# Kernel tuning notes

Measured on AMD Instinct MI355X. Metric: run time of the kernel, lower is better.

Reference implementation:

```python
import jax, jax.numpy as jnp
import numpy as np

B, S, IN_F, OUT_F = 4, 2048, 4096, 4096

def setup_inputs() -> dict:
    key = jax.random.key(0)
    k1, k2, k3 = jax.random.split(key, 3)
    # int8 activations and weights (symmetric range)
    x = jax.random.randint(k1, (B, S, IN_F), -128, 128, dtype=jnp.int32).astype(jnp.int8)
    weight_q = jax.random.randint(k2, (OUT_F, IN_F), -128, 128, dtype=jnp.int32).astype(jnp.int8)
    scale_x = jnp.float32(0.05)   # activation quant scale
    scale_w = jnp.float32(0.02)   # weight quant scale (scalar, per-tensor)
    scale_y = jax.random.uniform(k3, (OUT_F,), minval=0.5, maxval=2.0, dtype=jnp.float32)  # per-output-row scale
    return {"x": x, "weight_q": weight_q, "scale_x": scale_x, "scale_w": scale_w, "scale_y": scale_y}

def reference(x, weight_q, scale_x, scale_w, scale_y):
    # int8 GEMM with int32 accumulation: [B,S,IN] @ [OUT,IN]^T -> [B,S,OUT]
    acc = jax.lax.dot_general(x, weight_q, ((((2,), (1,)), ((), ()))),
                              preferred_element_type=jnp.int32)
    # fused requantization scale: scale_x * scale_w / scale_y  -> [OUT]
    requant_scale = (scale_x * scale_w / scale_y).astype(jnp.float32)
    out_f = acc.astype(jnp.float32) * requant_scale  # broadcast over last dim
    out_q = jnp.clip(jnp.round(out_f), -128, 127).astype(jnp.int8)
    return out_q, scale_y
```

## Files before the change

### kernel.cpp

```cpp
#include <hip/hip_runtime.h>
#include <cstdint>


#define MDIM 8192
#define NDIM 4096
#define KDIM 4096
#define BM 256
#define BN 256
#define NH 64

typedef int v4i __attribute__((ext_vector_type(4)));

#define FENCE() asm volatile("" ::: "memory")
#define BARX()                    \
  do {                            \
    FENCE();                      \
    __builtin_amdgcn_s_barrier(); \
    FENCE();                      \
  } while (0)
#define LGKM0() asm volatile("s_waitcnt lgkmcnt(0)" ::: "memory")
#define VMCNT4() asm volatile("s_waitcnt vmcnt(4)" ::: "memory")
#define VMCNT0() asm volatile("s_waitcnt vmcnt(0)" ::: "memory")

__device__ __forceinline__ uint32_t pack4(int a, int b, int c, int d) {
  return (uint32_t)(a & 0xFF) | ((uint32_t)(b & 0xFF) << 8) |
         ((uint32_t)(c & 0xFF) << 16) | ((uint32_t)(d & 0xFF) << 24);
}

__global__ __launch_bounds__(256) void pack_kernel(
    const int* __restrict__ x32, const int* __restrict__ w32,
    const float* __restrict__ sy, uint8_t* __restrict__ x8f,
    uint8_t* __restrict__ w8f, float* __restrict__ tail) {
  const int t = blockIdx.x * 256 + threadIdx.x;
  if (t < NDIM) tail[t] = sy[t];
  const int NXC = (MDIM / 16) * KDIM;
  const int NWC = (NDIM / 16) * KDIM;
  if (t >= NXC + NWC) return;
  const int* src;
  uint8_t* dst;
  int chunk;
  if (t < NXC) {
    chunk = t;
    src = x32;
    dst = x8f;
  } else {
    chunk = t - NXC;
    src = w32;
    dst = w8f;
  }
  const int lpos = chunk & 63;
  const int rf = (chunk >> 6) & 15;
  const int h = (chunk >> 10) & 63;
  const int mb = chunk >> 16;
  const int kl = lpos >> 4, fr = lpos & 15;
  const int r = mb * 256 + rf * 16 + fr;
  const int k0 = h * 64 + kl * 16;
  const int* s = src + (size_t)r * KDIM + k0;
  v4i a0 = *(const v4i*)(s + 0);
  v4i a1 = *(const v4i*)(s + 4);
  v4i a2 = *(const v4i*)(s + 8);
  v4i a3 = *(const v4i*)(s + 12);
  v4i o;
  o[0] = (int)pack4(a0[0], a0[1], a0[2], a0[3]);
  o[1] = (int)pack4(a1[0], a1[1], a1[2], a1[3]);
  o[2] = (int)pack4(a2[0], a2[1], a2[2], a2[3]);
  o[3] = (int)pack4(a3[0], a3[1], a3[2], a3[3]);
  *(v4i*)(dst + (size_t)chunk * 16) = o;
}

__global__ __launch_bounds__(512, 2) void gemm_kernel(
    const uint8_t* __restrict__ A8, const uint8_t* __restrict__ B8,
    const float* __restrict__ sxp, const float* __restrict__ swp,
    const float* __restrict__ syp, float* __restrict__ out) {
  __shared__ __align__(16) uint8_t lds[65536];

  const int tid = threadIdx.x;
  const int lane = tid & 63;
  const int wave = tid >> 6;

  const int wg = ((int)blockIdx.x % 8) * 64 + (int)blockIdx.x / 8;
  const int mb = wg >> 4;
  const int nb = wg & 15;

  const int wm2 = wave >> 2;
  const int wn4 = wave & 3;

  const uint8_t* Abase = A8 + ((size_t)mb << 20);
  const uint8_t* Bbase = B8 + ((size_t)nb << 20);

  const uint32_t tid16 = (uint32_t)tid * 16;
  const uint32_t lane16 = (uint32_t)lane * 16;
  const uint32_t aoff = ((uint32_t)(wm2 * 8) << 10) + lane16;
  const uint32_t boff = 16384u + ((uint32_t)(wn4 * 4) << 10) + lane16;

  v4i acc[8][4];
#pragma unroll
  for (int i = 0; i < 8; i++)
#pragma unroll
    for (int j = 0; j < 4; j++) acc[i][j] = (v4i){0, 0, 0, 0};

  auto gload = [&](const uint8_t* src, uint32_t ldsoff) {
    __builtin_amdgcn_global_load_lds(
        (const __attribute__((address_space(1))) void*)src,
        (__attribute__((address_space(3))) void*)(lds + ldsoff), 16, 0, 0);
  };
  auto stage = [&](int h) {
    const uint32_t lb = (uint32_t)(h & 1) * 32768u;
    const uint8_t* sa = Abase + ((size_t)h << 14) + tid16;
    const uint8_t* sb = Bbase + ((size_t)h << 14) + tid16;
    gload(sa, lb + tid16);
    gload(sa + 8192, lb + 8192u + tid16);
    gload(sb, lb + 16384u + tid16);
    gload(sb + 8192, lb + 24576u + tid16);
  };

  v4i af0[8], bf0[4], af1[8], bf1[4];

#define READ_FRAGS(AF, BF, SB)                                   \
  do {                                                           \
    _Pragma("unroll") for (int i = 0; i < 8; i++) AF[i] =        \
        *(const v4i*)(lds + (SB) + aoff + (i << 10));            \
    _Pragma("unroll") for (int j = 0; j < 4; j++) BF[j] =        \
        *(const v4i*)(lds + (SB) + boff + (j << 10));            \
  } while (0)

#define MFMA32(AF, BF)                                                        \
  do {                                                                        \
    _Pragma("unroll") for (int i = 0; i < 8; i++) _Pragma(                    \
        "unroll") for (int j = 0; j < 4; j++) acc[i][j] =                     \
        __builtin_amdgcn_mfma_i32_16x16x64_i8(AF[i], BF[j], acc[i][j], 0, 0, \
                                              0);                             \
  } while (0)

  stage(0);
  stage(1);
  VMCNT4();
  BARX();
  READ_FRAGS(af0, bf0, 0u);

  for (int h = 0; h < 62; h += 2) {
    LGKM0();
    BARX();
    stage(h + 2);
    VMCNT4();
    BARX();
    READ_FRAGS(af1, bf1, 32768u);
    MFMA32(af0, bf0);

    LGKM0();
    BARX();
    stage(h + 3);
    VMCNT4();
    BARX();
    READ_FRAGS(af0, bf0, 0u);
    MFMA32(af1, bf1);
  }

  LGKM0();
  BARX();
  VMCNT0();
  BARX();
  READ_FRAGS(af1, bf1, 32768u);
  MFMA32(af0, bf0);
  MFMA32(af1, bf1);

  const float s = sxp[0] * swp[0];
  const int kl = lane >> 4;
  const int fr = lane & 15;
  const int wrow = mb * 256 + wm2 * 128;
  const int wcol = nb * 256 + wn4 * 64;
#pragma unroll
  for (int j = 0; j < 4; j++) {
    const int col = wcol + j * 16 + fr;
    const float rs = s / syp[col];
#pragma unroll
    for (int i = 0; i < 8; i++) {
      const int row0 = wrow + i * 16 + kl * 4;
#pragma unroll
      for (int r = 0; r < 4; r++) {
        float v = rintf((float)acc[i][j][r] * rs);
        v = fminf(127.f, fmaxf(-128.f, v));
        out[(size_t)(row0 + r) * NDIM + col] = v;
      }
    }
  }
}

extern "C" void kernel_launch(void* const* d_in, const int* in_sizes, int n_in,
                              void* d_out, int out_size, void* d_ws, size_t ws_size,
                              hipStream_t stream) {
  const int* x32 = (const int*)d_in[0];
  const int* w32 = (const int*)d_in[1];
  const float* sx = (const float*)d_in[2];
  const float* sw = (const float*)d_in[3];
  const float* sy = (const float*)d_in[4];
  float* out = (float*)d_out;
  float* tail = out + (size_t)MDIM * NDIM;

  uint8_t* x8f = (uint8_t*)d_ws;
  uint8_t* w8f = x8f + (size_t)MDIM * KDIM;

  const int total = (MDIM / 16) * KDIM + (NDIM / 16) * KDIM;
  pack_kernel<<<total / 256, 256, 0, stream>>>(x32, w32, sy, x8f, w8f, tail);

  const int nblocks = (MDIM / BM) * (NDIM / BN);
  gemm_kernel<<<nblocks, 512, 0, stream>>>(x8f, w8f, sx, sw, sy, out);
}
```

Baseline: 184.2 us.

## Load A fragments directly from global to registers, pipeline B through four LDS stages

```diff
diff --git a/kernel.cpp b/kernel.cpp
--- a/kernel.cpp
+++ b/kernel.cpp
@@ -5,8 +5,6 @@
 #define MDIM 8192
 #define NDIM 4096
 #define KDIM 4096
-#define BM 256
-#define BN 256
 #define NH 64
 
 typedef int v4i __attribute__((ext_vector_type(4)));
@@ -18,9 +16,6 @@
     __builtin_amdgcn_s_barrier(); \
     FENCE();                      \
   } while (0)
-#define LGKM0() asm volatile("s_waitcnt lgkmcnt(0)" ::: "memory")
-#define VMCNT4() asm volatile("s_waitcnt vmcnt(4)" ::: "memory")
-#define VMCNT0() asm volatile("s_waitcnt vmcnt(0)" ::: "memory")
 
 __device__ __forceinline__ uint32_t pack4(int a, int b, int c, int d) {
   return (uint32_t)(a & 0xFF) | ((uint32_t)(b & 0xFF) << 8) |
@@ -85,13 +80,13 @@
   const int wm2 = wave >> 2;
   const int wn4 = wave & 3;
 
-  const uint8_t* Abase = A8 + ((size_t)mb << 20);
-  const uint8_t* Bbase = B8 + ((size_t)nb << 20);
+  const uint8_t* Apan = A8 + ((size_t)mb << 20) +
+                        ((uint32_t)(wm2 * 8) << 10) + (uint32_t)lane * 16;
+  const uint8_t* Bpan = B8 + ((size_t)nb << 20);
 
   const uint32_t tid16 = (uint32_t)tid * 16;
   const uint32_t lane16 = (uint32_t)lane * 16;
-  const uint32_t aoff = ((uint32_t)(wm2 * 8) << 10) + lane16;
-  const uint32_t boff = 16384u + ((uint32_t)(wn4 * 4) << 10) + lane16;
+  const uint32_t boff = ((uint32_t)(wn4 * 4) << 10) + lane16;
 
   v4i acc[8][4];
 #pragma unroll
@@ -104,65 +99,62 @@
         (const __attribute__((address_space(1))) void*)src,
         (__attribute__((address_space(3))) void*)(lds + ldsoff), 16, 0, 0);
   };
-  auto stage = [&](int h) {
-    const uint32_t lb = (uint32_t)(h & 1) * 32768u;
-    const uint8_t* sa = Abase + ((size_t)h << 14) + tid16;
-    const uint8_t* sb = Bbase + ((size_t)h << 14) + tid16;
-    gload(sa, lb + tid16);
-    gload(sa + 8192, lb + 8192u + tid16);
-    gload(sb, lb + 16384u + tid16);
-    gload(sb + 8192, lb + 24576u + tid16);
-  };
-
-  v4i af0[8], bf0[4], af1[8], bf1[4];
-
-#define READ_FRAGS(AF, BF, SB)                                   \
-  do {                                                           \
-    _Pragma("unroll") for (int i = 0; i < 8; i++) AF[i] =        \
-        *(const v4i*)(lds + (SB) + aoff + (i << 10));            \
-    _Pragma("unroll") for (int j = 0; j < 4; j++) BF[j] =        \
-        *(const v4i*)(lds + (SB) + boff + (j << 10));            \
-  } while (0)
+  auto stageB = [&](int h) {
+    const uint32_t s = ((uint32_t)h & 3u) * 16384u;
+    const uint8_t* src = Bpan + ((size_t)h << 14) + tid16;
+    gload(src, s + tid16);
+    gload(src + 8192, s + 8192u + tid16);
+  };
+  auto loadA = [&](v4i(&a)[8], int h) {
+    const uint8_t* p = Apan + ((size_t)h << 14);
+#pragma unroll
+    for (int i = 0; i < 8; i++) a[i] = *(const v4i*)(p + (i << 10));
+  };
+  auto readB = [&](v4i(&b)[4], int h) {
+    const uint8_t* L = lds + ((uint32_t)h & 3u) * 16384u + boff;
+#pragma unroll
+    for (int j = 0; j < 4; j++) b[j] = *(const v4i*)(L + (j << 10));
+  };
 
 #define MFMA32(AF, BF)                                                        \
   do {                                                                        \
     _Pragma("unroll") for (int i = 0; i < 8; i++) _Pragma(                    \
         "unroll") for (int j = 0; j < 4; j++) acc[i][j] =                     \
-        __builtin_amdgcn_mfma_i32_16x16x64_i8(AF[i], BF[j], acc[i][j], 0, 0, \
+        __builtin_amdgcn_mfma_i32_16x16x64_i8(AF[i], BF[j], acc[i][j], 0, 0,  \
                                               0);                             \
   } while (0)
 
-  stage(0);
-  stage(1);
-  VMCNT4();
+  v4i aX[8], aY[8], bX[4], bY[4];
+
+  stageB(0);
+  stageB(1);
+  stageB(2);
+  loadA(aX, 0);
+  asm volatile("s_waitcnt vmcnt(12)" ::: "memory");
   BARX();
-  READ_FRAGS(af0, bf0, 0u);
+  readB(bX, 0);
 
   for (int h = 0; h < 62; h += 2) {
-    LGKM0();
+    asm volatile("s_waitcnt vmcnt(10)" ::: "memory");
     BARX();
-    stage(h + 2);
-    VMCNT4();
+    stageB(h + 3);
+    loadA(aY, h + 1);
+    readB(bY, h + 1);
+    MFMA32(aX, bX);
+
+    asm volatile("s_waitcnt vmcnt(10)" ::: "memory");
     BARX();
-    READ_FRAGS(af1, bf1, 32768u);
-    MFMA32(af0, bf0);
-
-    LGKM0();
-    BARX();
-    stage(h + 3);
-    VMCNT4();
-    BARX();
-    READ_FRAGS(af0, bf0, 0u);
-    MFMA32(af1, bf1);
+    if (h + 4 < NH) stageB(h + 4);
+    loadA(aX, h + 2);
+    readB(bX, h + 2);
+    MFMA32(aY, bY);
   }
-
-  LGKM0();
+  asm volatile("s_waitcnt vmcnt(8)" ::: "memory");
   BARX();
-  VMCNT0();
-  BARX();
-  READ_FRAGS(af1, bf1, 32768u);
-  MFMA32(af0, bf0);
-  MFMA32(af1, bf1);
+  loadA(aY, 63);
+  readB(bY, 63);
+  MFMA32(aX, bX);
+  MFMA32(aY, bY);
 
   const float s = sxp[0] * swp[0];
   const int kl = lane >> 4;
@@ -203,6 +195,6 @@
   const int total = (MDIM / 16) * KDIM + (NDIM / 16) * KDIM;
   pack_kernel<<<total / 256, 256, 0, stream>>>(x32, w32, sy, x8f, w8f, tail);
 
-  const int nblocks = (MDIM / BM) * (NDIM / BN);
+  const int nblocks = (MDIM / 256) * (NDIM / 256);
   gemm_kernel<<<nblocks, 512, 0, stream>>>(x8f, w8f, sx, sw, sy, out);
 }
```

Result: slower. 205.0 us (+11.3%).
